# Kernel tuning notes

Measured on AMD Instinct MI355X. Metric: run time of the kernel, lower is better.

Reference implementation:

```python
import jax, jax.numpy as jnp
import numpy as np

D = 128            # actual_dim / embed_dim
DM = 2 * D         # d_model
HID = 2 * DM       # LSTMCell hidden size
NSYM = 200000
PAD = NSYM
B = 4096
S = 5
NB = 64
STEPS = 4
EPS = 1e-6


def setup_inputs() -> dict:
    key = jax.random.key(0)
    ks = jax.random.split(key, 24)
    def rn(k, sh, scale=0.02):
        return jax.random.normal(k, sh, dtype=jnp.float32) * scale
    emb = rn(ks[10], (NSYM + 1, D)).at[PAD].set(0.0)  # padding row zeroed
    inp = {
        'query': jax.random.randint(ks[0], (B, 2), 0, NSYM),
        'support': jax.random.randint(ks[1], (S, 2), 0, NSYM),
        'q_l_conn': jax.random.randint(ks[2], (B, NB, 2), 0, NSYM),
        'q_l_deg': jax.random.randint(ks[3], (B,), 0, NB),
        'q_r_conn': jax.random.randint(ks[4], (B, NB, 2), 0, NSYM),
        'q_r_deg': jax.random.randint(ks[5], (B,), 0, NB),
        's_l_conn': jax.random.randint(ks[6], (S, NB, 2), 0, NSYM),
        's_l_deg': jax.random.randint(ks[7], (S,), 0, NB),
        's_r_conn': jax.random.randint(ks[8], (S, NB, 2), 0, NSYM),
        's_r_deg': jax.random.randint(ks[9], (S,), 0, NB),
        'emb': emb,
        'gcn_w': rn(ks[11], (D, 2 * D)),
        'gcn_bias': jnp.zeros((D,), jnp.float32),
        'proj1_w': rn(ks[12], (2 * DM, DM)),
        'proj1_b': jnp.zeros((2 * DM,), jnp.float32),
        'proj2_w': rn(ks[13], (DM, 2 * DM)),
        'proj2_b': jnp.zeros((DM,), jnp.float32),
        'ln_g': jnp.ones((DM,), jnp.float32),
        'ln_b': jnp.zeros((DM,), jnp.float32),
        'w_ih': rn(ks[14], (4 * HID, DM)),
        'w_hh': rn(ks[15], (4 * HID, HID)),
        'b_ih': jnp.zeros((4 * HID,), jnp.float32),
        'b_hh': jnp.zeros((4 * HID,), jnp.float32),
    }
    return inp


def _neighbor_encoder(conn, deg, emb, gcn_w, gcn_bias):
    # conn: [N, NB, 2] ids (rel, ent); deg: [N]
    rel = emb[conn[:, :, 0]]                     # [N, NB, D] gather
    ent = emb[conn[:, :, 1]]                     # [N, NB, D] gather
    x = jnp.concatenate([rel, ent], axis=-1)     # [N, NB, 2D]
    out = jnp.einsum('bnd,kd->bnk', x, gcn_w) + gcn_bias  # [N, NB, D]
    denom = jnp.maximum(deg, 1).astype(out.dtype)[:, None]
    return jnp.tanh(out.sum(axis=1) / denom)     # [N, D]


def _support_encoder(x, proj1_w, proj1_b, proj2_w, proj2_b, ln_g, ln_b):
    residual = x
    h = jax.nn.relu(x @ proj1_w.T + proj1_b)
    h = h @ proj2_w.T + proj2_b
    z = h + residual
    mu = z.mean(axis=-1, keepdims=True)
    sigma = jnp.std(z, axis=-1, keepdims=True, ddof=1)
    return ln_g * (z - mu) / (sigma + EPS) + ln_b


def _query_encoder(support_vec, query, w_ih, w_hh, b_ih, b_hh):
    # support_vec: [DM] (single support prototype); query: [B, DM]
    bsz = query.shape[0]
    h_r = jnp.zeros((bsz, HID), query.dtype)
    c = jnp.zeros((bsz, HID), query.dtype)
    xW = query @ w_ih.T + b_ih  # invariant across steps
    h = query
    for _ in range(STEPS):
        gates = xW + h_r @ w_hh.T + b_hh
        i, f, g, o = jnp.split(gates, 4, axis=-1)
        c = jax.nn.sigmoid(f) * c + jax.nn.sigmoid(i) * jnp.tanh(g)
        h_cell = jax.nn.sigmoid(o) * jnp.tanh(c)
        h = query + h_cell[:, :DM]
        # attention over a single support row: softmax of one logit == 1
        r = jnp.broadcast_to(support_vec[None, :], h.shape)
        h_r = jnp.concatenate([h, r], axis=-1)
    return h


def reference(query, support, q_l_conn, q_l_deg, q_r_conn, q_r_deg,
              s_l_conn, s_l_deg, s_r_conn, s_r_deg,
              emb, gcn_w, gcn_bias, proj1_w, proj1_b, proj2_w, proj2_b,
              ln_g, ln_b, w_ih, w_hh, b_ih, b_hh):
    ql = _neighbor_encoder(q_l_conn, q_l_deg, emb, gcn_w, gcn_bias)
    qr = _neighbor_encoder(q_r_conn, q_r_deg, emb, gcn_w, gcn_bias)
    sl = _neighbor_encoder(s_l_conn, s_l_deg, emb, gcn_w, gcn_bias)
    sr = _neighbor_encoder(s_r_conn, s_r_deg, emb, gcn_w, gcn_bias)
    query_nb = jnp.concatenate([ql, qr], axis=-1)    # [B, DM]
    support_nb = jnp.concatenate([sl, sr], axis=-1)  # [S, DM]
    se = lambda x: _support_encoder(x, proj1_w, proj1_b, proj2_w, proj2_b, ln_g, ln_b)
    support_g = se(support_nb).mean(axis=0)          # [DM]
    query_g = se(query_nb)                            # [B, DM]
    query_f = _query_encoder(support_g, query_g, w_ih, w_hh, b_ih, b_hh)
    qn = query_f / jnp.maximum(jnp.linalg.norm(query_f, axis=-1, keepdims=True), 1e-12)
    sn = support_g / jnp.maximum(jnp.linalg.norm(support_g), 1e-12)
    return qn @ sn                                    # [B] matching scores
```

## Files before the change

### kernel.cpp

```cpp
#include <hip/hip_runtime.h>

#define BQ 4096
#define NS 5

typedef __attribute__((ext_vector_type(8))) short bf16x8;
typedef __attribute__((ext_vector_type(4))) float f32x4;
typedef unsigned short ushortT;

#define WS_QNB    0
#define WS_Z      1048576
#define WS_QG     2097152
#define WS_XW     3145728
#define WS_CBUF   5242880
#define WS_XS     6291456
#define WS_H1B    7348224
#define WS_ABF    7872512
#define WS_HB1    8134656
#define WS_P1B    8396800
#define WS_P2B    8462336
#define WS_WIHB   8527872
#define WS_WHHB   8658944
#define WS_GWB    8790016
#define WS_SNB    8806400
#define WS_H1G    8807680
#define WS_ZB     8810240
#define WS_SG     8811520
#define WS_SN     8811776
#define WS_SWL    8812032
#define WS_BL     8813056

__device__ __forceinline__ float wave_allreduce(float v) {
#pragma unroll
  for (int off = 32; off > 0; off >>= 1) v += __shfl_xor(v, off, 64);
  return v;
}
__device__ __forceinline__ float block_allreduce(float v, float* buf) {
  v = wave_allreduce(v);
  __syncthreads();
  if ((threadIdx.x & 63) == 0) buf[threadIdx.x >> 6] = v;
  __syncthreads();
  return buf[0] + buf[1] + buf[2] + buf[3];
}
__device__ __forceinline__ float sigm(float x) { return 1.0f / (1.0f + expf(-x)); }
__device__ __forceinline__ ushortT f2bf(float f) {
  unsigned int u = __float_as_uint(f);
  unsigned int r = (u + 0x7fffu + ((u >> 16) & 1u)) >> 16;
  return (ushortT)r;
}
__device__ __forceinline__ float bf2f(ushortT u) {
  return __uint_as_float(((unsigned int)u) << 16);
}
__device__ __forceinline__ float dot4(float4 a, float4 b) {
  return a.x * b.x + a.y * b.y + a.z * b.z + a.w * b.w;
}

__global__ void k_pack(const float* __restrict__ w_ih, const float* __restrict__ w_hh,
                       const float* __restrict__ p1w, const float* __restrict__ p2w,
                       const float* __restrict__ gcn_w,
                       const float* __restrict__ b_ih, const float* __restrict__ b_hh,
                       ushortT* __restrict__ p1b16, ushortT* __restrict__ p2b16,
                       ushortT* __restrict__ wihb, ushortT* __restrict__ whhb,
                       ushortT* __restrict__ gwb, float* __restrict__ bL) {
  const int stride = gridDim.x * blockDim.x;
  const int gid = blockIdx.x * blockDim.x + threadIdx.x;
  for (int i = gid; i < 131072; i += stride) p1b16[i] = f2bf(p1w[i]);
  for (int i = gid; i < 131072; i += stride) p2b16[i] = f2bf(p2w[i]);
  for (int i = gid; i < 262144; i += stride) {
    int n = i >> 8, k = i & 255;
    int j = (n >> 2) + 512 * (n & 3);
    wihb[i] = f2bf(w_ih[j * 256 + k]);
    whhb[i] = f2bf(w_hh[j * 512 + k]);
  }
  for (int i = gid; i < 32768; i += stride) gwb[i] = f2bf(gcn_w[i]);
  for (int i = gid; i < 1024; i += stride) {
    int j = (i >> 2) + 512 * (i & 3);
    bL[i] = b_ih[j] + b_hh[j];
  }
}

__global__ __launch_bounds__(256) void k_gather(
    const int* __restrict__ qlc, const int* __restrict__ qrc,
    const int* __restrict__ slc, const int* __restrict__ src_,
    const float* __restrict__ emb, ushortT* __restrict__ XS) {
  const int r = blockIdx.x;
  const int b = r >> 1, side = r & 1;
  const int t = threadIdx.x;
  const int* cg;
  if (b < BQ) cg = (side ? qrc : qlc) + (size_t)b * 128;
  else        cg = (side ? src_ : slc) + (size_t)(b - BQ) * 128;
  __shared__ int connS[128];
  __shared__ __align__(16) float part[8][132];
  if (t < 128) connS[t] = cg[t];
  __syncthreads();
  const int s = t >> 5, l = t & 31;
  const float4* emb4 = (const float4*)emb;
  float4 acc = make_float4(0.f, 0.f, 0.f, 0.f);
#pragma unroll
  for (int kb = 0; kb < 2; kb++) {
    int im[8];
#pragma unroll
    for (int k = 0; k < 8; k++) im[k] = connS[(kb * 8 + k) * 8 + s];
    float4 v[8];
#pragma unroll
    for (int k = 0; k < 8; k++) v[k] = emb4[(size_t)im[k] * 32 + l];
#pragma unroll
    for (int k = 0; k < 8; k++) {
      acc.x += v[k].x; acc.y += v[k].y; acc.z += v[k].z; acc.w += v[k].w;
    }
  }
  *(float4*)&part[s][l * 4] = acc;
  __syncthreads();
  const int hf = t >> 7, dd = t & 127;
  float sum = part[hf][dd] + part[2 + hf][dd] + part[4 + hf][dd] + part[6 + hf][dd];
  XS[(size_t)r * 256 + t] = f2bf(sum);
}

__global__ __launch_bounds__(256) void k_gcn(
    const ushortT* __restrict__ XS, const ushortT* __restrict__ gwb,
    const float* __restrict__ gcn_bias,
    const int* __restrict__ qld, const int* __restrict__ qrd,
    const int* __restrict__ sld, const int* __restrict__ srd,
    float* __restrict__ qnb, float* __restrict__ snb, ushortT* __restrict__ xq) {
  __shared__ short As[64 * 40];
  __shared__ short Bs[128 * 40];
  __shared__ int degl[32], degr[32];
  const int t = threadIdx.x;
  const int row0 = blockIdx.x * 64;
  if (t < 32) {
    int b = (row0 >> 1) + t;
    int dl = 1, dr = 1;
    if (b < BQ) { dl = qld[b]; dr = qrd[b]; }
    else if (b < BQ + NS) { dl = sld[b - BQ]; dr = srd[b - BQ]; }
    degl[t] = (dl > 0) ? dl : 1;
    degr[t] = (dr > 0) ? dr : 1;
  }
  const int wave = t >> 6, lane = t & 63;
  const int wm = wave >> 1, wn = wave & 1, quad = lane >> 4, mr = lane & 15;
  f32x4 acc[2][4];
#pragma unroll
  for (int mi = 0; mi < 2; mi++)
#pragma unroll
    for (int ni = 0; ni < 4; ni++) acc[mi][ni] = (f32x4){0.f, 0.f, 0.f, 0.f};
  const int arow = t >> 2, akc = t & 3;
  for (int k0 = 0; k0 < 256; k0 += 32) {
    float4 av = *(const float4*)(XS + (size_t)(row0 + arow) * 256 + k0 + akc * 8);
    float4 bv0 = *(const float4*)(gwb + (size_t)arow * 256 + k0 + akc * 8);
    float4 bv1 = *(const float4*)(gwb + (size_t)(64 + arow) * 256 + k0 + akc * 8);
    __syncthreads();
    *(float4*)&As[arow * 40 + akc * 8] = av;
    *(float4*)&Bs[arow * 40 + akc * 8] = bv0;
    *(float4*)&Bs[(64 + arow) * 40 + akc * 8] = bv1;
    __syncthreads();
    bf16x8 af[2], bfr[4];
#pragma unroll
    for (int mi = 0; mi < 2; mi++)
      af[mi] = *(const bf16x8*)&As[(wm * 32 + mi * 16 + mr) * 40 + quad * 8];
#pragma unroll
    for (int ni = 0; ni < 4; ni++)
      bfr[ni] = *(const bf16x8*)&Bs[(wn * 64 + ni * 16 + mr) * 40 + quad * 8];
#pragma unroll
    for (int mi = 0; mi < 2; mi++)
#pragma unroll
      for (int ni = 0; ni < 4; ni++)
        acc[mi][ni] = __builtin_amdgcn_mfma_f32_16x16x32_bf16(af[mi], bfr[ni], acc[mi][ni], 0, 0, 0);
  }
#pragma unroll
  for (int mi = 0; mi < 2; mi++) {
#pragma unroll
    for (int ni = 0; ni < 4; ni++) {
      const int col = wn * 64 + ni * 16 + mr;
      const int rb = row0 + wm * 32 + mi * 16 + quad * 4;
      const float bs = 64.0f * gcn_bias[col];
#pragma unroll
      for (int reg = 0; reg < 4; reg++) {
        const int row = rb + reg;
        const int b = row >> 1, side = row & 1;
        if (b >= BQ + NS) continue;
        const int li = (row >> 1) - (row0 >> 1);
        const int deg = side ? degr[li] : degl[li];
        float val = tanhf((acc[mi][ni][reg] + bs) / (float)deg);
        if (b < BQ) {
          const size_t o = (size_t)b * 256 + side * 128 + col;
          qnb[o] = val;
          xq[o] = f2bf(val);
        } else {
          snb[(size_t)(b - BQ) * 256 + side * 128 + col] = val;
        }
      }
    }
  }
}

__global__ __launch_bounds__(256) void k_sup1(
    const float* __restrict__ snb, const float* __restrict__ p1w,
    const float* __restrict__ p1b, float* __restrict__ h1g) {
  const int w = blockIdx.x * 4 + (threadIdx.x >> 6);
  const int lane = threadIdx.x & 63;
  const int r = w >> 9, j = w & 511;
  float4 x = *(const float4*)&snb[r * 256 + lane * 4];
  float4 wv = *(const float4*)&p1w[(size_t)j * 256 + lane * 4];
  float s = wave_allreduce(dot4(x, wv));
  if (lane == 0) h1g[r * 512 + j] = fmaxf(s + p1b[j], 0.f);
}

__global__ __launch_bounds__(256) void k_sup2(
    const float* __restrict__ snb, const float* __restrict__ h1g,
    const float* __restrict__ p2w, const float* __restrict__ p2b,
    float* __restrict__ zb) {
  const int w = blockIdx.x * 4 + (threadIdx.x >> 6);
  const int lane = threadIdx.x & 63;
  const int r = w >> 8, tt = w & 255;
  float4 h0 = *(const float4*)&h1g[r * 512 + lane * 4];
  float4 h1 = *(const float4*)&h1g[r * 512 + 256 + lane * 4];
  float4 w0 = *(const float4*)&p2w[(size_t)tt * 512 + lane * 4];
  float4 w1 = *(const float4*)&p2w[(size_t)tt * 512 + 256 + lane * 4];
  float s = wave_allreduce(dot4(h0, w0) + dot4(h1, w1));
  if (lane == 0) zb[r * 256 + tt] = s + p2b[tt] + snb[r * 256 + tt];
}

__global__ __launch_bounds__(256) void k_sup3(
    const float* __restrict__ zb, const float* __restrict__ ln_g,
    const float* __restrict__ ln_b, float* __restrict__ sg, float* __restrict__ sn) {
  const int t = threadIdx.x;
  __shared__ float rbuf[4];
  float acc = 0.f;
  for (int r = 0; r < NS; r++) {
    float z = zb[r * 256 + t];
    float s = block_allreduce(z, rbuf);
    float mu = s * (1.f / 256.f);
    float dz = z - mu;
    float s2 = block_allreduce(dz * dz, rbuf);
    float rstd = 1.f / (sqrtf(s2 * (1.f / 255.f)) + 1e-6f);
    acc += ln_g[t] * dz * rstd + ln_b[t];
    __syncthreads();
  }
  float g = acc * (1.f / (float)NS);
  sg[t] = g;
  float n2 = block_allreduce(g * g, rbuf);
  sn[t] = g / fmaxf(sqrtf(n2), 1e-12f);
}

__global__ __launch_bounds__(256) void k_sup4(
    const float* __restrict__ sg, const float* __restrict__ w_hh,
    float* __restrict__ sWl) {
  const int n = blockIdx.x * 4 + (threadIdx.x >> 6);
  const int lane = threadIdx.x & 63;
  const int j = (n >> 2) + 512 * (n & 3);
  float4 x = *(const float4*)&sg[lane * 4];
  float4 wv = *(const float4*)&w_hh[(size_t)j * 512 + 256 + lane * 4];
  float s = wave_allreduce(dot4(x, wv));
  if (lane == 0) sWl[n] = s;
}

__global__ __launch_bounds__(256) void k_gemm(
    const ushortT* __restrict__ A, const ushortT* __restrict__ B,
    const float* __restrict__ bias, const float* __restrict__ aux,
    float* __restrict__ outf, ushortT* __restrict__ outb,
    int K, int N, int nbn, int mode) {
  __shared__ short As[64 * 40];
  __shared__ short Bs[128 * 40];
  const int t = threadIdx.x;
  const int bn = blockIdx.x % nbn, bm = blockIdx.x / nbn;
  const int row0 = bm * 64, col0 = bn * 128;
  const int wave = t >> 6, lane = t & 63;
  const int wm = wave >> 1, wn = wave & 1, quad = lane >> 4, mr = lane & 15;
  f32x4 acc[2][4];
#pragma unroll
  for (int mi = 0; mi < 2; mi++)
#pragma unroll
    for (int ni = 0; ni < 4; ni++) acc[mi][ni] = (f32x4){0.f, 0.f, 0.f, 0.f};
  const int arow = t >> 2, akc = t & 3;
  for (int k0 = 0; k0 < K; k0 += 32) {
    float4 av = *(const float4*)(A + (size_t)(row0 + arow) * K + k0 + akc * 8);
    float4 bv0 = *(const float4*)(B + (size_t)(col0 + arow) * K + k0 + akc * 8);
    float4 bv1 = *(const float4*)(B + (size_t)(col0 + 64 + arow) * K + k0 + akc * 8);
    __syncthreads();
    *(float4*)&As[arow * 40 + akc * 8] = av;
    *(float4*)&Bs[arow * 40 + akc * 8] = bv0;
    *(float4*)&Bs[(64 + arow) * 40 + akc * 8] = bv1;
    __syncthreads();
    bf16x8 af[2], bfr[4];
#pragma unroll
    for (int mi = 0; mi < 2; mi++)
      af[mi] = *(const bf16x8*)&As[(wm * 32 + mi * 16 + mr) * 40 + quad * 8];
#pragma unroll
    for (int ni = 0; ni < 4; ni++)
      bfr[ni] = *(const bf16x8*)&Bs[(wn * 64 + ni * 16 + mr) * 40 + quad * 8];
#pragma unroll
    for (int mi = 0; mi < 2; mi++)
#pragma unroll
      for (int ni = 0; ni < 4; ni++)
        acc[mi][ni] = __builtin_amdgcn_mfma_f32_16x16x32_bf16(af[mi], bfr[ni], acc[mi][ni], 0, 0, 0);
  }
#pragma unroll
  for (int mi = 0; mi < 2; mi++) {
#pragma unroll
    for (int ni = 0; ni < 4; ni++) {
      const int col = col0 + wn * 64 + ni * 16 + mr;
      const int rb = row0 + wm * 32 + mi * 16 + quad * 4;
      const float bs = bias[col];
#pragma unroll
      for (int reg = 0; reg < 4; reg++) {
        const int row = rb + reg;
        const size_t off = (size_t)row * N + col;
        float v = acc[mi][ni][reg];
        if (mode == 0) outb[off] = f2bf(fmaxf(v + bs, 0.f));
        else outf[off] = v + bs + aux[off];
      }
    }
  }
}

__global__ __launch_bounds__(256) void k_gemm_lstm(
    const ushortT* __restrict__ A, const ushortT* __restrict__ B,
    const float* __restrict__ bL, const float* __restrict__ sWl,
    const float* __restrict__ qg, ushortT* __restrict__ xwb,
    float* __restrict__ cbuf, ushortT* __restrict__ hb_out, int phase) {
  __shared__ short As[64 * 40];
  __shared__ short Bs[128 * 40];
  __shared__ __align__(16) float Cs[64 * 132];
  const int t = threadIdx.x;
  const int bn = blockIdx.x & 7, bm = blockIdx.x >> 3;
  const int row0 = bm * 64, col0 = bn * 128;
  const int wave = t >> 6, lane = t & 63;
  const int wm = wave >> 1, wn = wave & 1, quad = lane >> 4, mr = lane & 15;
  f32x4 acc[2][4];
#pragma unroll
  for (int mi = 0; mi < 2; mi++)
#pragma unroll
    for (int ni = 0; ni < 4; ni++) acc[mi][ni] = (f32x4){0.f, 0.f, 0.f, 0.f};
  const int arow = t >> 2, akc = t & 3;
  for (int k0 = 0; k0 < 256; k0 += 32) {
    float4 av = *(const float4*)(A + (size_t)(row0 + arow) * 256 + k0 + akc * 8);
    float4 bv0 = *(const float4*)(B + (size_t)(col0 + arow) * 256 + k0 + akc * 8);
    float4 bv1 = *(const float4*)(B + (size_t)(col0 + 64 + arow) * 256 + k0 + akc * 8);
    __syncthreads();
    *(float4*)&As[arow * 40 + akc * 8] = av;
    *(float4*)&Bs[arow * 40 + akc * 8] = bv0;
    *(float4*)&Bs[(64 + arow) * 40 + akc * 8] = bv1;
    __syncthreads();
    bf16x8 af[2], bfr[4];
#pragma unroll
    for (int mi = 0; mi < 2; mi++)
      af[mi] = *(const bf16x8*)&As[(wm * 32 + mi * 16 + mr) * 40 + quad * 8];
#pragma unroll
    for (int ni = 0; ni < 4; ni++)
      bfr[ni] = *(const bf16x8*)&Bs[(wn * 64 + ni * 16 + mr) * 40 + quad * 8];
#pragma unroll
    for (int mi = 0; mi < 2; mi++)
#pragma unroll
      for (int ni = 0; ni < 4; ni++)
        acc[mi][ni] = __builtin_amdgcn_mfma_f32_16x16x32_bf16(af[mi], bfr[ni], acc[mi][ni], 0, 0, 0);
  }
#pragma unroll
  for (int mi = 0; mi < 2; mi++)
#pragma unroll
    for (int ni = 0; ni < 4; ni++)
#pragma unroll
      for (int reg = 0; reg < 4; reg++)
        Cs[(wm * 32 + mi * 16 + quad * 4 + reg) * 132 + wn * 64 + ni * 16 + mr] =
            acc[mi][ni][reg];
  __syncthreads();
  const int u = t & 31, grp = t >> 5;
  const int ugl = bn * 32 + u;
#pragma unroll
  for (int i = 0; i < 8; i++) {
    const int rl = grp * 8 + i;
    const int row = row0 + rl;
    const size_t o = (size_t)row * 256 + ugl;
    float4 gv = *(const float4*)&Cs[rl * 132 + u * 4];
    if (phase == 0) {
      float4 bb = *(const float4*)&bL[col0 + u * 4];
      gv.x += bb.x; gv.y += bb.y; gv.z += bb.z; gv.w += bb.w;
      float c0 = sigm(gv.x) * tanhf(gv.z);
      float h = qg[o] + sigm(gv.w) * tanhf(c0);
      cbuf[o] = c0;
      hb_out[o] = f2bf(h);
      float4 sv = *(const float4*)&sWl[col0 + u * 4];
      ushort4 xo;
      xo.x = f2bf(gv.x + sv.x); xo.y = f2bf(gv.y + sv.y);
      xo.z = f2bf(gv.z + sv.z); xo.w = f2bf(gv.w + sv.w);
      *(ushort4*)&xwb[(size_t)row * 1024 + col0 + u * 4] = xo;
    } else {
      ushort4 xv = *(const ushort4*)&xwb[(size_t)row * 1024 + col0 + u * 4];
      gv.x += bf2f(xv.x); gv.y += bf2f(xv.y);
      gv.z += bf2f(xv.z); gv.w += bf2f(xv.w);
      float c = sigm(gv.y) * cbuf[o] + sigm(gv.x) * tanhf(gv.z);
      float h = qg[o] + sigm(gv.w) * tanhf(c);
      if (phase == 2) {
        cbuf[o] = h;
      } else {
        cbuf[o] = c;
        hb_out[o] = f2bf(h);
      }
    }
  }
}

__global__ __launch_bounds__(256) void k_ln(
    const float* __restrict__ Z, const float* __restrict__ ln_g,
    const float* __restrict__ ln_b, float* __restrict__ qg, ushortT* __restrict__ qgb) {
  const int t = threadIdx.x;
  const int row = blockIdx.x * 4 + (t >> 6);
  const int lane = t & 63;
  float4 z = *(const float4*)&Z[(size_t)row * 256 + lane * 4];
  float s = wave_allreduce(z.x + z.y + z.z + z.w);
  float mu = s * (1.f / 256.f);
  float dx = z.x - mu, dy = z.y - mu, dz = z.z - mu, dw = z.w - mu;
  float s2 = wave_allreduce(dx * dx + dy * dy + dz * dz + dw * dw);
  float rstd = 1.f / (sqrtf(s2 * (1.f / 255.f)) + 1e-6f);
  float4 g = *(const float4*)&ln_g[lane * 4];
  float4 bb = *(const float4*)&ln_b[lane * 4];
  float4 o;
  o.x = g.x * dx * rstd + bb.x;
  o.y = g.y * dy * rstd + bb.y;
  o.z = g.z * dz * rstd + bb.z;
  o.w = g.w * dw * rstd + bb.w;
  *(float4*)&qg[(size_t)row * 256 + lane * 4] = o;
  ushort4 u;
  u.x = f2bf(o.x); u.y = f2bf(o.y); u.z = f2bf(o.z); u.w = f2bf(o.w);
  *(ushort4*)&qgb[(size_t)row * 256 + lane * 4] = u;
}

__global__ __launch_bounds__(256) void k_out(
    const float* __restrict__ hf, const float* __restrict__ sn, float* __restrict__ out) {
  const int t = threadIdx.x;
  const int row = blockIdx.x * 4 + (t >> 6);
  const int lane = t & 63;
  float4 h = *(const float4*)&hf[(size_t)row * 256 + lane * 4];
  float4 s = *(const float4*)&sn[lane * 4];
  float dt = wave_allreduce(dot4(h, s));
  float nr = wave_allreduce(dot4(h, h));
  if (lane == 0) out[row] = dt / fmaxf(sqrtf(nr), 1e-12f);
}

extern "C" void kernel_launch(void* const* d_in, const int* in_sizes, int n_in,
                              void* d_out, int out_size, void* d_ws, size_t ws_size,
                              hipStream_t stream) {
  const int* q_l_conn = (const int*)d_in[2];
  const int* q_l_deg  = (const int*)d_in[3];
  const int* q_r_conn = (const int*)d_in[4];
  const int* q_r_deg  = (const int*)d_in[5];
  const int* s_l_conn = (const int*)d_in[6];
  const int* s_l_deg  = (const int*)d_in[7];
  const int* s_r_conn = (const int*)d_in[8];
  const int* s_r_deg  = (const int*)d_in[9];
  const float* emb      = (const float*)d_in[10];
  const float* gcn_w    = (const float*)d_in[11];
  const float* gcn_bias = (const float*)d_in[12];
  const float* proj1_w  = (const float*)d_in[13];
  const float* proj1_b  = (const float*)d_in[14];
  const float* proj2_w  = (const float*)d_in[15];
  const float* proj2_b  = (const float*)d_in[16];
  const float* ln_g     = (const float*)d_in[17];
  const float* ln_b     = (const float*)d_in[18];
  const float* w_ih     = (const float*)d_in[19];
  const float* w_hh     = (const float*)d_in[20];
  const float* b_ih     = (const float*)d_in[21];
  const float* b_hh     = (const float*)d_in[22];

  float* ws = (float*)d_ws;
  float* qnb   = ws + WS_QNB;
  float* Z     = ws + WS_Z;
  float* qg    = ws + WS_QG;
  ushortT* xwb = (ushortT*)(ws + WS_XW);
  float* cbuf  = ws + WS_CBUF;
  ushortT* XS    = (ushortT*)(ws + WS_XS);
  ushortT* h1b   = (ushortT*)(ws + WS_H1B);
  ushortT* abf   = (ushortT*)(ws + WS_ABF);
  ushortT* hb1   = (ushortT*)(ws + WS_HB1);
  ushortT* p1b16 = (ushortT*)(ws + WS_P1B);
  ushortT* p2b16 = (ushortT*)(ws + WS_P2B);
  ushortT* wihb  = (ushortT*)(ws + WS_WIHB);
  ushortT* whhb  = (ushortT*)(ws + WS_WHHB);
  ushortT* gwb   = (ushortT*)(ws + WS_GWB);
  float* snb   = ws + WS_SNB;
  float* h1g   = ws + WS_H1G;
  float* zb    = ws + WS_ZB;
  float* sg    = ws + WS_SG;
  float* sn    = ws + WS_SN;
  float* sWl   = ws + WS_SWL;
  float* bL    = ws + WS_BL;
  float* out   = (float*)d_out;

  hipLaunchKernelGGL(k_pack, dim3(512), dim3(256), 0, stream,
                     w_ih, w_hh, proj1_w, proj2_w, gcn_w, b_ih, b_hh,
                     p1b16, p2b16, wihb, whhb, gwb, bL);
  hipLaunchKernelGGL(k_gather, dim3(2 * (BQ + NS)), dim3(256), 0, stream,
                     q_l_conn, q_r_conn, s_l_conn, s_r_conn, emb, XS);
  hipLaunchKernelGGL(k_gcn, dim3(129), dim3(256), 0, stream,
                     XS, gwb, gcn_bias, q_l_deg, q_r_deg, s_l_deg, s_r_deg,
                     qnb, snb, abf);
  hipLaunchKernelGGL(k_sup1, dim3(640), dim3(256), 0, stream, snb, proj1_w, proj1_b, h1g);
  hipLaunchKernelGGL(k_sup2, dim3(320), dim3(256), 0, stream, snb, h1g, proj2_w, proj2_b, zb);
  hipLaunchKernelGGL(k_sup3, dim3(1), dim3(256), 0, stream, zb, ln_g, ln_b, sg, sn);
  hipLaunchKernelGGL(k_sup4, dim3(256), dim3(256), 0, stream, sg, w_hh, sWl);
  hipLaunchKernelGGL(k_gemm, dim3(64 * 4), dim3(256), 0, stream,
                     abf, p1b16, proj1_b, (const float*)nullptr, (float*)nullptr, h1b,
                     256, 512, 4, 0);
  hipLaunchKernelGGL(k_gemm, dim3(64 * 2), dim3(256), 0, stream,
                     h1b, p2b16, proj2_b, qnb, Z, (ushortT*)nullptr,
                     512, 256, 2, 1);
  hipLaunchKernelGGL(k_ln, dim3(BQ / 4), dim3(256), 0, stream, Z, ln_g, ln_b, qg, abf);
  hipLaunchKernelGGL(k_gemm_lstm, dim3(512), dim3(256), 0, stream,
                     abf, wihb, bL, sWl, qg, xwb, cbuf, hb1, 0);
  hipLaunchKernelGGL(k_gemm_lstm, dim3(512), dim3(256), 0, stream,
                     hb1, whhb, bL, sWl, qg, xwb, cbuf, abf, 1);
  hipLaunchKernelGGL(k_gemm_lstm, dim3(512), dim3(256), 0, stream,
                     abf, whhb, bL, sWl, qg, xwb, cbuf, hb1, 1);
  hipLaunchKernelGGL(k_gemm_lstm, dim3(512), dim3(256), 0, stream,
                     hb1, whhb, bL, sWl, qg, xwb, cbuf, (ushortT*)nullptr, 2);
  hipLaunchKernelGGL(k_out, dim3(BQ / 4), dim3(256), 0, stream, cbuf, sn, out);
}
```

Measured before the change: 364.0 us.

## Merge support-path kernels into query GEMM launches as extra blocks

The weight packing kernel is folded into the gather launch, and each small support-set kernel (proj1, proj2, layernorm/mean, sWl) becomes extra trailing blocks of the matching query-path launch. This cuts the number of kernel launches from 15 to 10 and lets the tiny support work run alongside the big query work. The sWl support-bias term is no longer folded into xwb in phase 0. It is now added in phases 1 and 2, because sWl is computed by the same launch as phase 0. This adds branch divergence per block and extra kernel parameters, and slightly changes the order of rounding.

```diff
diff --git a/kernel.cpp b/kernel.cpp
--- a/kernel.cpp
+++ b/kernel.cpp
@@ -54,37 +54,38 @@
   return a.x * b.x + a.y * b.y + a.z * b.z + a.w * b.w;
 }
 
-__global__ void k_pack(const float* __restrict__ w_ih, const float* __restrict__ w_hh,
-                       const float* __restrict__ p1w, const float* __restrict__ p2w,
-                       const float* __restrict__ gcn_w,
-                       const float* __restrict__ b_ih, const float* __restrict__ b_hh,
-                       ushortT* __restrict__ p1b16, ushortT* __restrict__ p2b16,
-                       ushortT* __restrict__ wihb, ushortT* __restrict__ whhb,
-                       ushortT* __restrict__ gwb, float* __restrict__ bL) {
-  const int stride = gridDim.x * blockDim.x;
-  const int gid = blockIdx.x * blockDim.x + threadIdx.x;
-  for (int i = gid; i < 131072; i += stride) p1b16[i] = f2bf(p1w[i]);
-  for (int i = gid; i < 131072; i += stride) p2b16[i] = f2bf(p2w[i]);
-  for (int i = gid; i < 262144; i += stride) {
-    int n = i >> 8, k = i & 255;
-    int j = (n >> 2) + 512 * (n & 3);
-    wihb[i] = f2bf(w_ih[j * 256 + k]);
-    whhb[i] = f2bf(w_hh[j * 512 + k]);
-  }
-  for (int i = gid; i < 32768; i += stride) gwb[i] = f2bf(gcn_w[i]);
-  for (int i = gid; i < 1024; i += stride) {
-    int j = (i >> 2) + 512 * (i & 3);
-    bL[i] = b_ih[j] + b_hh[j];
-  }
-}
-
 __global__ __launch_bounds__(256) void k_gather(
     const int* __restrict__ qlc, const int* __restrict__ qrc,
     const int* __restrict__ slc, const int* __restrict__ src_,
-    const float* __restrict__ emb, ushortT* __restrict__ XS) {
+    const float* __restrict__ emb, ushortT* __restrict__ XS,
+    const float* __restrict__ w_ih, const float* __restrict__ w_hh,
+    const float* __restrict__ p1w, const float* __restrict__ p2w,
+    const float* __restrict__ gcn_w,
+    const float* __restrict__ b_ih, const float* __restrict__ b_hh,
+    ushortT* __restrict__ p1b16, ushortT* __restrict__ p2b16,
+    ushortT* __restrict__ wihb, ushortT* __restrict__ whhb,
+    ushortT* __restrict__ gwb, float* __restrict__ bL) {
   const int r = blockIdx.x;
+  const int t = threadIdx.x;
+  if (r >= 2 * (BQ + NS)) {
+    const int gid = (r - 2 * (BQ + NS)) * 256 + t;
+    const int stride = 512 * 256;
+    for (int i = gid; i < 131072; i += stride) p1b16[i] = f2bf(p1w[i]);
+    for (int i = gid; i < 131072; i += stride) p2b16[i] = f2bf(p2w[i]);
+    for (int i = gid; i < 262144; i += stride) {
+      int n = i >> 8, k = i & 255;
+      int j = (n >> 2) + 512 * (n & 3);
+      wihb[i] = f2bf(w_ih[j * 256 + k]);
+      whhb[i] = f2bf(w_hh[j * 512 + k]);
+    }
+    for (int i = gid; i < 32768; i += stride) gwb[i] = f2bf(gcn_w[i]);
+    for (int i = gid; i < 1024; i += stride) {
+      int j = (i >> 2) + 512 * (i & 3);
+      bL[i] = b_ih[j] + b_hh[j];
+    }
+    return;
+  }
   const int b = r >> 1, side = r & 1;
-  const int t = threadIdx.x;
   const int* cg;
   if (b < BQ) cg = (side ? qrc : qlc) + (size_t)b * 128;
   else        cg = (side ? src_ : slc) + (size_t)(b - BQ) * 128;
@@ -191,136 +192,25 @@
   }
 }
 
-__global__ __launch_bounds__(256) void k_sup1(
+__global__ __launch_bounds__(256) void k_proj1(
+    const ushortT* __restrict__ A, const ushortT* __restrict__ B,
+    const float* __restrict__ bias, ushortT* __restrict__ outb,
     const float* __restrict__ snb, const float* __restrict__ p1w,
     const float* __restrict__ p1b, float* __restrict__ h1g) {
-  const int w = blockIdx.x * 4 + (threadIdx.x >> 6);
-  const int lane = threadIdx.x & 63;
-  const int r = w >> 9, j = w & 511;
-  float4 x = *(const float4*)&snb[r * 256 + lane * 4];
-  float4 wv = *(const float4*)&p1w[(size_t)j * 256 + lane * 4];
-  float s = wave_allreduce(dot4(x, wv));
-  if (lane == 0) h1g[r * 512 + j] = fmaxf(s + p1b[j], 0.f);
-}
-
-__global__ __launch_bounds__(256) void k_sup2(
-    const float* __restrict__ snb, const float* __restrict__ h1g,
-    const float* __restrict__ p2w, const float* __restrict__ p2b,
-    float* __restrict__ zb) {
-  const int w = blockIdx.x * 4 + (threadIdx.x >> 6);
-  const int lane = threadIdx.x & 63;
-  const int r = w >> 8, tt = w & 255;
-  float4 h0 = *(const float4*)&h1g[r * 512 + lane * 4];
-  float4 h1 = *(const float4*)&h1g[r * 512 + 256 + lane * 4];
-  float4 w0 = *(const float4*)&p2w[(size_t)tt * 512 + lane * 4];
-  float4 w1 = *(const float4*)&p2w[(size_t)tt * 512 + 256 + lane * 4];
-  float s = wave_allreduce(dot4(h0, w0) + dot4(h1, w1));
-  if (lane == 0) zb[r * 256 + tt] = s + p2b[tt] + snb[r * 256 + tt];
-}
-
-__global__ __launch_bounds__(256) void k_sup3(
-    const float* __restrict__ zb, const float* __restrict__ ln_g,
-    const float* __restrict__ ln_b, float* __restrict__ sg, float* __restrict__ sn) {
-  const int t = threadIdx.x;
-  __shared__ float rbuf[4];
-  float acc = 0.f;
-  for (int r = 0; r < NS; r++) {
-    float z = zb[r * 256 + t];
-    float s = block_allreduce(z, rbuf);
-    float mu = s * (1.f / 256.f);
-    float dz = z - mu;
-    float s2 = block_allreduce(dz * dz, rbuf);
-    float rstd = 1.f / (sqrtf(s2 * (1.f / 255.f)) + 1e-6f);
-    acc += ln_g[t] * dz * rstd + ln_b[t];
-    __syncthreads();
-  }
-  float g = acc * (1.f / (float)NS);
-  sg[t] = g;
-  float n2 = block_allreduce(g * g, rbuf);
-  sn[t] = g / fmaxf(sqrtf(n2), 1e-12f);
-}
-
-__global__ __launch_bounds__(256) void k_sup4(
-    const float* __restrict__ sg, const float* __restrict__ w_hh,
-    float* __restrict__ sWl) {
-  const int n = blockIdx.x * 4 + (threadIdx.x >> 6);
-  const int lane = threadIdx.x & 63;
-  const int j = (n >> 2) + 512 * (n & 3);
-  float4 x = *(const float4*)&sg[lane * 4];
-  float4 wv = *(const float4*)&w_hh[(size_t)j * 512 + 256 + lane * 4];
-  float s = wave_allreduce(dot4(x, wv));
-  if (lane == 0) sWl[n] = s;
-}
-
-__global__ __launch_bounds__(256) void k_gemm(
-    const ushortT* __restrict__ A, const ushortT* __restrict__ B,
-    const float* __restrict__ bias, const float* __restrict__ aux,
-    float* __restrict__ outf, ushortT* __restrict__ outb,
-    int K, int N, int nbn, int mode) {
   __shared__ short As[64 * 40];
   __shared__ short Bs[128 * 40];
   const int t = threadIdx.x;
-  const int bn = blockIdx.x % nbn, bm = blockIdx.x / nbn;
-  const int row0 = bm * 64, col0 = bn * 128;
-  const int wave = t >> 6, lane = t & 63;
-  const int wm = wave >> 1, wn = wave & 1, quad = lane >> 4, mr = lane & 15;
-  f32x4 acc[2][4];
-#pragma unroll
-  for (int mi = 0; mi < 2; mi++)
-#pragma unroll
-    for (int ni = 0; ni < 4; ni++) acc[mi][ni] = (f32x4){0.f, 0.f, 0.f, 0.f};
-  const int arow = t >> 2, akc = t & 3;
-  for (int k0 = 0; k0 < K; k0 += 32) {
-    float4 av = *(const float4*)(A + (size_t)(row0 + arow) * K + k0 + akc * 8);
-    float4 bv0 = *(const float4*)(B + (size_t)(col0 + arow) * K + k0 + akc * 8);
-    float4 bv1 = *(const float4*)(B + (size_t)(col0 + 64 + arow) * K + k0 + akc * 8);
-    __syncthreads();
-    *(float4*)&As[arow * 40 + akc * 8] = av;
-    *(float4*)&Bs[arow * 40 + akc * 8] = bv0;
-    *(float4*)&Bs[(64 + arow) * 40 + akc * 8] = bv1;
-    __syncthreads();
-    bf16x8 af[2], bfr[4];
-#pragma unroll
-    for (int mi = 0; mi < 2; mi++)
-      af[mi] = *(const bf16x8*)&As[(wm * 32 + mi * 16 + mr) * 40 + quad * 8];
-#pragma unroll
-    for (int ni = 0; ni < 4; ni++)
-      bfr[ni] = *(const bf16x8*)&Bs[(wn * 64 + ni * 16 + mr) * 40 + quad * 8];
-#pragma unroll
-    for (int mi = 0; mi < 2; mi++)
-#pragma unroll
-      for (int ni = 0; ni < 4; ni++)
-        acc[mi][ni] = __builtin_amdgcn_mfma_f32_16x16x32_bf16(af[mi], bfr[ni], acc[mi][ni], 0, 0, 0);
-  }
-#pragma unroll
-  for (int mi = 0; mi < 2; mi++) {
-#pragma unroll
-    for (int ni = 0; ni < 4; ni++) {
-      const int col = col0 + wn * 64 + ni * 16 + mr;
-      const int rb = row0 + wm * 32 + mi * 16 + quad * 4;
-      const float bs = bias[col];
-#pragma unroll
-      for (int reg = 0; reg < 4; reg++) {
-        const int row = rb + reg;
-        const size_t off = (size_t)row * N + col;
-        float v = acc[mi][ni][reg];
-        if (mode == 0) outb[off] = f2bf(fmaxf(v + bs, 0.f));
-        else outf[off] = v + bs + aux[off];
-      }
-    }
-  }
-}
-
-__global__ __launch_bounds__(256) void k_gemm_lstm(
-    const ushortT* __restrict__ A, const ushortT* __restrict__ B,
-    const float* __restrict__ bL, const float* __restrict__ sWl,
-    const float* __restrict__ qg, ushortT* __restrict__ xwb,
-    float* __restrict__ cbuf, ushortT* __restrict__ hb_out, int phase) {
-  __shared__ short As[64 * 40];
-  __shared__ short Bs[128 * 40];
-  __shared__ __align__(16) float Cs[64 * 132];
-  const int t = threadIdx.x;
-  const int bn = blockIdx.x & 7, bm = blockIdx.x >> 3;
+  if (blockIdx.x >= 256) {
+    const int w = (blockIdx.x - 256) * 4 + (t >> 6);
+    const int lane = t & 63;
+    const int r = w >> 9, j = w & 511;
+    float4 x = *(const float4*)&snb[r * 256 + lane * 4];
+    float4 wv = *(const float4*)&p1w[(size_t)j * 256 + lane * 4];
+    float s = wave_allreduce(dot4(x, wv));
+    if (lane == 0) h1g[r * 512 + j] = fmaxf(s + p1b[j], 0.f);
+    return;
+  }
+  const int bn = blockIdx.x % 4, bm = blockIdx.x / 4;
   const int row0 = bm * 64, col0 = bn * 128;
   const int wave = t >> 6, lane = t & 63;
   const int wm = wave >> 1, wn = wave & 1, quad = lane >> 4, mr = lane & 15;
@@ -353,54 +243,116 @@
         acc[mi][ni] = __builtin_amdgcn_mfma_f32_16x16x32_bf16(af[mi], bfr[ni], acc[mi][ni], 0, 0, 0);
   }
 #pragma unroll
+  for (int mi = 0; mi < 2; mi++) {
+#pragma unroll
+    for (int ni = 0; ni < 4; ni++) {
+      const int col = col0 + wn * 64 + ni * 16 + mr;
+      const int rb = row0 + wm * 32 + mi * 16 + quad * 4;
+      const float bs = bias[col];
+#pragma unroll
+      for (int reg = 0; reg < 4; reg++) {
+        const int row = rb + reg;
+        outb[(size_t)row * 512 + col] = f2bf(fmaxf(acc[mi][ni][reg] + bs, 0.f));
+      }
+    }
+  }
+}
+
+__global__ __launch_bounds__(256) void k_proj2(
+    const ushortT* __restrict__ A, const ushortT* __restrict__ B,
+    const float* __restrict__ bias, const float* __restrict__ aux,
+    float* __restrict__ outf,
+    const float* __restrict__ snb, const float* __restrict__ h1g,
+    const float* __restrict__ p2w, const float* __restrict__ p2b,
+    float* __restrict__ zb) {
+  __shared__ short As[64 * 40];
+  __shared__ short Bs[128 * 40];
+  const int t = threadIdx.x;
+  if (blockIdx.x >= 128) {
+    const int w = (blockIdx.x - 128) * 4 + (t >> 6);
+    const int lane = t & 63;
+    const int r = w >> 8, tt = w & 255;
+    float4 h0 = *(const float4*)&h1g[r * 512 + lane * 4];
+    float4 h1 = *(const float4*)&h1g[r * 512 + 256 + lane * 4];
+    float4 w0 = *(const float4*)&p2w[(size_t)tt * 512 + lane * 4];
+    float4 w1 = *(const float4*)&p2w[(size_t)tt * 512 + 256 + lane * 4];
+    float s = wave_allreduce(dot4(h0, w0) + dot4(h1, w1));
+    if (lane == 0) zb[r * 256 + tt] = s + p2b[tt] + snb[r * 256 + tt];
+    return;
+  }
+  const int bn = blockIdx.x % 2, bm = blockIdx.x / 2;
+  const int row0 = bm * 64, col0 = bn * 128;
+  const int wave = t >> 6, lane = t & 63;
+  const int wm = wave >> 1, wn = wave & 1, quad = lane >> 4, mr = lane & 15;
+  f32x4 acc[2][4];
+#pragma unroll
   for (int mi = 0; mi < 2; mi++)
 #pragma unroll
+    for (int ni = 0; ni < 4; ni++) acc[mi][ni] = (f32x4){0.f, 0.f, 0.f, 0.f};
+  const int arow = t >> 2, akc = t & 3;
+  for (int k0 = 0; k0 < 512; k0 += 32) {
+    float4 av = *(const float4*)(A + (size_t)(row0 + arow) * 512 + k0 + akc * 8);
+    float4 bv0 = *(const float4*)(B + (size_t)(col0 + arow) * 512 + k0 + akc * 8);
+    float4 bv1 = *(const float4*)(B + (size_t)(col0 + 64 + arow) * 512 + k0 + akc * 8);
+    __syncthreads();
+    *(float4*)&As[arow * 40 + akc * 8] = av;
+    *(float4*)&Bs[arow * 40 + akc * 8] = bv0;
+    *(float4*)&Bs[(64 + arow) * 40 + akc * 8] = bv1;
+    __syncthreads();
+    bf16x8 af[2], bfr[4];
+#pragma unroll
+    for (int mi = 0; mi < 2; mi++)
+      af[mi] = *(const bf16x8*)&As[(wm * 32 + mi * 16 + mr) * 40 + quad * 8];
+#pragma unroll
     for (int ni = 0; ni < 4; ni++)
-#pragma unroll
-      for (int reg = 0; reg < 4; reg++)
-        Cs[(wm * 32 + mi * 16 + quad * 4 + reg) * 132 + wn * 64 + ni * 16 + mr] =
-            acc[mi][ni][reg];
-  __syncthreads();
-  const int u = t & 31, grp = t >> 5;
-  const int ugl = bn * 32 + u;
-#pragma unroll
-  for (int i = 0; i < 8; i++) {
-    const int rl = grp * 8 + i;
-    const int row = row0 + rl;
-    const size_t o = (size_t)row * 256 + ugl;
-    float4 gv = *(const float4*)&Cs[rl * 132 + u * 4];
-    if (phase == 0) {
-      float4 bb = *(const float4*)&bL[col0 + u * 4];
-      gv.x += bb.x; gv.y += bb.y; gv.z += bb.z; gv.w += bb.w;
-      float c0 = sigm(gv.x) * tanhf(gv.z);
-      float h = qg[o] + sigm(gv.w) * tanhf(c0);
-      cbuf[o] = c0;
-      hb_out[o] = f2bf(h);
-      float4 sv = *(const float4*)&sWl[col0 + u * 4];
-      ushort4 xo;
-      xo.x = f2bf(gv.x + sv.x); xo.y = f2bf(gv.y + sv.y);
-      xo.z = f2bf(gv.z + sv.z); xo.w = f2bf(gv.w + sv.w);
-      *(ushort4*)&xwb[(size_t)row * 1024 + col0 + u * 4] = xo;
-    } else {
-      ushort4 xv = *(const ushort4*)&xwb[(size_t)row * 1024 + col0 + u * 4];
-      gv.x += bf2f(xv.x); gv.y += bf2f(xv.y);
-      gv.z += bf2f(xv.z); gv.w += bf2f(xv.w);
-      float c = sigm(gv.y) * cbuf[o] + sigm(gv.x) * tanhf(gv.z);
-      float h = qg[o] + sigm(gv.w) * tanhf(c);
-      if (phase == 2) {
-        cbuf[o] = h;
-      } else {
-        cbuf[o] = c;
-        hb_out[o] = f2bf(h);
+      bfr[ni] = *(const bf16x8*)&Bs[(wn * 64 + ni * 16 + mr) * 40 + quad * 8];
+#pragma unroll
+    for (int mi = 0; mi < 2; mi++)
+#pragma unroll
+      for (int ni = 0; ni < 4; ni++)
+        acc[mi][ni] = __builtin_amdgcn_mfma_f32_16x16x32_bf16(af[mi], bfr[ni], acc[mi][ni], 0, 0, 0);
+  }
+#pragma unroll
+  for (int mi = 0; mi < 2; mi++) {
+#pragma unroll
+    for (int ni = 0; ni < 4; ni++) {
+      const int col = col0 + wn * 64 + ni * 16 + mr;
+      const int rb = row0 + wm * 32 + mi * 16 + quad * 4;
+      const float bs = bias[col];
+#pragma unroll
+      for (int reg = 0; reg < 4; reg++) {
+        const int row = rb + reg;
+        const size_t off = (size_t)row * 256 + col;
+        outf[off] = acc[mi][ni][reg] + bs + aux[off];
       }
     }
   }
 }
 
-__global__ __launch_bounds__(256) void k_ln(
+__global__ __launch_bounds__(256) void k_ln2(
     const float* __restrict__ Z, const float* __restrict__ ln_g,
-    const float* __restrict__ ln_b, float* __restrict__ qg, ushortT* __restrict__ qgb) {
-  const int t = threadIdx.x;
+    const float* __restrict__ ln_b, float* __restrict__ qg, ushortT* __restrict__ qgb,
+    const float* __restrict__ zb, float* __restrict__ sg, float* __restrict__ sn_out) {
+  const int t = threadIdx.x;
+  if (blockIdx.x >= BQ / 4) {
+    __shared__ float rbuf[4];
+    float acc = 0.f;
+    for (int r = 0; r < NS; r++) {
+      float z = zb[r * 256 + t];
+      float s = block_allreduce(z, rbuf);
+      float mu = s * (1.f / 256.f);
+      float dz = z - mu;
+      float s2 = block_allreduce(dz * dz, rbuf);
+      float rstd = 1.f / (sqrtf(s2 * (1.f / 255.f)) + 1e-6f);
+      acc += ln_g[t] * dz * rstd + ln_b[t];
+      __syncthreads();
+    }
+    float g = acc * (1.f / (float)NS);
+    sg[t] = g;
+    float n2 = block_allreduce(g * g, rbuf);
+    sn_out[t] = g / fmaxf(sqrtf(n2), 1e-12f);
+    return;
+  }
   const int row = blockIdx.x * 4 + (t >> 6);
   const int lane = t & 63;
   float4 z = *(const float4*)&Z[(size_t)row * 256 + lane * 4];
@@ -420,6 +372,103 @@
   ushort4 u;
   u.x = f2bf(o.x); u.y = f2bf(o.y); u.z = f2bf(o.z); u.w = f2bf(o.w);
   *(ushort4*)&qgb[(size_t)row * 256 + lane * 4] = u;
+}
+
+__global__ __launch_bounds__(256) void k_gemm_lstm(
+    const ushortT* __restrict__ A, const ushortT* __restrict__ B,
+    const float* __restrict__ bL, float* __restrict__ sWl,
+    const float* __restrict__ qg, ushortT* __restrict__ xwb,
+    float* __restrict__ cbuf, ushortT* __restrict__ hb_out,
+    const float* __restrict__ sg, const float* __restrict__ w_hh, int phase) {
+  __shared__ short As[64 * 40];
+  __shared__ short Bs[128 * 40];
+  __shared__ __align__(16) float Cs[64 * 132];
+  const int t = threadIdx.x;
+  if (blockIdx.x >= 512) {
+    const int n = (blockIdx.x - 512) * 4 + (t >> 6);
+    const int lane = t & 63;
+    const int j = (n >> 2) + 512 * (n & 3);
+    float4 x = *(const float4*)&sg[lane * 4];
+    float4 wv = *(const float4*)&w_hh[(size_t)j * 512 + 256 + lane * 4];
+    float s = wave_allreduce(dot4(x, wv));
+    if (lane == 0) sWl[n] = s;
+    return;
+  }
+  const int bn = blockIdx.x & 7, bm = blockIdx.x >> 3;
+  const int row0 = bm * 64, col0 = bn * 128;
+  const int wave = t >> 6, lane = t & 63;
+  const int wm = wave >> 1, wn = wave & 1, quad = lane >> 4, mr = lane & 15;
+  f32x4 acc[2][4];
+#pragma unroll
+  for (int mi = 0; mi < 2; mi++)
+#pragma unroll
+    for (int ni = 0; ni < 4; ni++) acc[mi][ni] = (f32x4){0.f, 0.f, 0.f, 0.f};
+  const int arow = t >> 2, akc = t & 3;
+  for (int k0 = 0; k0 < 256; k0 += 32) {
+    float4 av = *(const float4*)(A + (size_t)(row0 + arow) * 256 + k0 + akc * 8);
+    float4 bv0 = *(const float4*)(B + (size_t)(col0 + arow) * 256 + k0 + akc * 8);
+    float4 bv1 = *(const float4*)(B + (size_t)(col0 + 64 + arow) * 256 + k0 + akc * 8);
+    __syncthreads();
+    *(float4*)&As[arow * 40 + akc * 8] = av;
+    *(float4*)&Bs[arow * 40 + akc * 8] = bv0;
+    *(float4*)&Bs[(64 + arow) * 40 + akc * 8] = bv1;
+    __syncthreads();
+    bf16x8 af[2], bfr[4];
+#pragma unroll
+    for (int mi = 0; mi < 2; mi++)
+      af[mi] = *(const bf16x8*)&As[(wm * 32 + mi * 16 + mr) * 40 + quad * 8];
+#pragma unroll
+    for (int ni = 0; ni < 4; ni++)
+      bfr[ni] = *(const bf16x8*)&Bs[(wn * 64 + ni * 16 + mr) * 40 + quad * 8];
+#pragma unroll
+    for (int mi = 0; mi < 2; mi++)
+#pragma unroll
+      for (int ni = 0; ni < 4; ni++)
+        acc[mi][ni] = __builtin_amdgcn_mfma_f32_16x16x32_bf16(af[mi], bfr[ni], acc[mi][ni], 0, 0, 0);
+  }
+#pragma unroll
+  for (int mi = 0; mi < 2; mi++)
+#pragma unroll
+    for (int ni = 0; ni < 4; ni++)
+#pragma unroll
+      for (int reg = 0; reg < 4; reg++)
+        Cs[(wm * 32 + mi * 16 + quad * 4 + reg) * 132 + wn * 64 + ni * 16 + mr] =
+            acc[mi][ni][reg];
+  __syncthreads();
+  const int u = t & 31, grp = t >> 5;
+  const int ugl = bn * 32 + u;
+#pragma unroll
+  for (int i = 0; i < 8; i++) {
+    const int rl = grp * 8 + i;
+    const int row = row0 + rl;
+    const size_t o = (size_t)row * 256 + ugl;
+    float4 gv = *(const float4*)&Cs[rl * 132 + u * 4];
+    if (phase == 0) {
+      float4 bb = *(const float4*)&bL[col0 + u * 4];
+      gv.x += bb.x; gv.y += bb.y; gv.z += bb.z; gv.w += bb.w;
+      float c0 = sigm(gv.x) * tanhf(gv.z);
+      float h = qg[o] + sigm(gv.w) * tanhf(c0);
+      cbuf[o] = c0;
+      hb_out[o] = f2bf(h);
+      ushort4 xo;
+      xo.x = f2bf(gv.x); xo.y = f2bf(gv.y);
+      xo.z = f2bf(gv.z); xo.w = f2bf(gv.w);
+      *(ushort4*)&xwb[(size_t)row * 1024 + col0 + u * 4] = xo;
+    } else {
+      ushort4 xv = *(const ushort4*)&xwb[(size_t)row * 1024 + col0 + u * 4];
+      float4 sv = *(const float4*)&sWl[col0 + u * 4];
+      gv.x += bf2f(xv.x) + sv.x; gv.y += bf2f(xv.y) + sv.y;
+      gv.z += bf2f(xv.z) + sv.z; gv.w += bf2f(xv.w) + sv.w;
+      float c = sigm(gv.y) * cbuf[o] + sigm(gv.x) * tanhf(gv.z);
+      float h = qg[o] + sigm(gv.w) * tanhf(c);
+      if (phase == 2) {
+        cbuf[o] = h;
+      } else {
+        cbuf[o] = c;
+        hb_out[o] = f2bf(h);
+      }
+    }
+  }
 }
 
 __global__ __launch_bounds__(256) void k_out(
@@ -483,32 +532,28 @@
   float* bL    = ws + WS_BL;
   float* out   = (float*)d_out;
 
-  hipLaunchKernelGGL(k_pack, dim3(512), dim3(256), 0, stream,
+  hipLaunchKernelGGL(k_gather, dim3(2 * (BQ + NS) + 512), dim3(256), 0, stream,
+                     q_l_conn, q_r_conn, s_l_conn, s_r_conn, emb, XS,
                      w_ih, w_hh, proj1_w, proj2_w, gcn_w, b_ih, b_hh,
                      p1b16, p2b16, wihb, whhb, gwb, bL);
-  hipLaunchKernelGGL(k_gather, dim3(2 * (BQ + NS)), dim3(256), 0, stream,
-                     q_l_conn, q_r_conn, s_l_conn, s_r_conn, emb, XS);
   hipLaunchKernelGGL(k_gcn, dim3(129), dim3(256), 0, stream,
                      XS, gwb, gcn_bias, q_l_deg, q_r_deg, s_l_deg, s_r_deg,
                      qnb, snb, abf);
-  hipLaunchKernelGGL(k_sup1, dim3(640), dim3(256), 0, stream, snb, proj1_w, proj1_b, h1g);
-  hipLaunchKernelGGL(k_sup2, dim3(320), dim3(256), 0, stream, snb, h1g, proj2_w, proj2_b, zb);
-  hipLaunchKernelGGL(k_sup3, dim3(1), dim3(256), 0, stream, zb, ln_g, ln_b, sg, sn);
-  hipLaunchKernelGGL(k_sup4, dim3(256), dim3(256), 0, stream, sg, w_hh, sWl);
-  hipLaunchKernelGGL(k_gemm, dim3(64 * 4), dim3(256), 0, stream,
-                     abf, p1b16, proj1_b, (const float*)nullptr, (float*)nullptr, h1b,
-                     256, 512, 4, 0);
-  hipLaunchKernelGGL(k_gemm, dim3(64 * 2), dim3(256), 0, stream,
-                     h1b, p2b16, proj2_b, qnb, Z, (ushortT*)nullptr,
-                     512, 256, 2, 1);
-  hipLaunchKernelGGL(k_ln, dim3(BQ / 4), dim3(256), 0, stream, Z, ln_g, ln_b, qg, abf);
+  hipLaunchKernelGGL(k_proj1, dim3(256 + 640), dim3(256), 0, stream,
+                     abf, p1b16, proj1_b, h1b,
+                     snb, proj1_w, proj1_b, h1g);
+  hipLaunchKernelGGL(k_proj2, dim3(128 + 320), dim3(256), 0, stream,
+                     h1b, p2b16, proj2_b, qnb, Z,
+                     snb, h1g, proj2_w, proj2_b, zb);
+  hipLaunchKernelGGL(k_ln2, dim3(BQ / 4 + 1), dim3(256), 0, stream,
+                     Z, ln_g, ln_b, qg, abf, zb, sg, sn);
+  hipLaunchKernelGGL(k_gemm_lstm, dim3(512 + 256), dim3(256), 0, stream,
+                     abf, wihb, bL, sWl, qg, xwb, cbuf, hb1, sg, w_hh, 0);
   hipLaunchKernelGGL(k_gemm_lstm, dim3(512), dim3(256), 0, stream,
-                     abf, wihb, bL, sWl, qg, xwb, cbuf, hb1, 0);
+                     hb1, whhb, bL, sWl, qg, xwb, cbuf, abf, sg, w_hh, 1);
   hipLaunchKernelGGL(k_gemm_lstm, dim3(512), dim3(256), 0, stream,
-                     hb1, whhb, bL, sWl, qg, xwb, cbuf, abf, 1);
+                     abf, whhb, bL, sWl, qg, xwb, cbuf, hb1, sg, w_hh, 1);
   hipLaunchKernelGGL(k_gemm_lstm, dim3(512), dim3(256), 0, stream,
-                     abf, whhb, bL, sWl, qg, xwb, cbuf, hb1, 1);
-  hipLaunchKernelGGL(k_gemm_lstm, dim3(512), dim3(256), 0, stream,
-                     hb1, whhb, bL, sWl, qg, xwb, cbuf, (ushortT*)nullptr, 2);
+                     hb1, whhb, bL, sWl, qg, xwb, cbuf, (ushortT*)nullptr, sg, w_hh, 2);
   hipLaunchKernelGGL(k_out, dim3(BQ / 4), dim3(256), 0, stream, cbuf, sn, out);
 }
```

New measurement: 335.8 us. 7.8% less time.
